# Kernel tuning notes

Hardware: AMD Instinct MI355X
Metric: run time of the kernel (lower is better)

The kernel has to match this reference:

```python
import jax, jax.numpy as jnp
import numpy as np

R = 32
GN_GROUPS = 8
GN_EPS = 1e-5


def group_norm(x, gamma, beta, groups=GN_GROUPS, eps=GN_EPS):
    B, C = x.shape[0], x.shape[1]
    sp = x.shape[2:]
    xg = x.reshape(B, groups, -1)
    mean = xg.mean(-1, keepdims=True)
    var = xg.var(-1, keepdims=True)
    xg = (xg - mean) * jax.lax.rsqrt(var + eps)
    x = xg.reshape((B, C) + sp)
    bshape = (1, C) + (1,) * len(sp)
    return x * gamma.reshape(bshape) + beta.reshape(bshape)


def swish(x):
    return x * jax.nn.sigmoid(x)


def voxelize_coords(coords, r):
    # coords: [B,3,N] -> normalized coords in [0, r-1]
    nc = coords - coords.mean(2, keepdims=True)
    scale = jnp.linalg.norm(nc, axis=1, keepdims=True).max(axis=2, keepdims=True) * 2.0
    nc = nc / scale + 0.5
    return jnp.clip(nc * r, 0.0, r - 1.0)


def avg_voxelize(features, vox, r):
    # features [B,C,N], vox int32 [B,3,N] -> [B,C,r,r,r] scatter-mean
    B, C, N = features.shape
    flat = (vox[:, 0] * r + vox[:, 1]) * r + vox[:, 2]          # [B,N]
    seg = (flat + jnp.arange(B, dtype=flat.dtype)[:, None] * (r ** 3)).reshape(-1)
    feats = features.transpose(0, 2, 1).reshape(B * N, C)
    sums = jax.ops.segment_sum(feats, seg, num_segments=B * r ** 3)
    cnts = jax.ops.segment_sum(jnp.ones((B * N,), features.dtype), seg,
                               num_segments=B * r ** 3)
    mean = sums / jnp.maximum(cnts, 1.0)[:, None]
    return mean.reshape(B, r, r, r, C).transpose(0, 4, 1, 2, 3)


def trilinear_devoxelize(grid, coords, r):
    # grid [B,C,r,r,r], coords float [B,3,N] in [0,r-1] -> [B,C,N]
    B, C = grid.shape[0], grid.shape[1]
    N = coords.shape[2]
    lo = jnp.floor(coords).astype(jnp.int32)                     # [B,3,N]
    frac = coords - lo.astype(coords.dtype)
    hi = jnp.minimum(lo + 1, r - 1)
    gridf = grid.reshape(B, C, r * r * r)
    out = jnp.zeros((B, C, N), grid.dtype)
    for dx in (0, 1):
        for dy in (0, 1):
            for dz in (0, 1):
                ix = hi[:, 0] if dx else lo[:, 0]
                iy = hi[:, 1] if dy else lo[:, 1]
                iz = hi[:, 2] if dz else lo[:, 2]
                wx = frac[:, 0] if dx else (1.0 - frac[:, 0])
                wy = frac[:, 1] if dy else (1.0 - frac[:, 1])
                wz = frac[:, 2] if dz else (1.0 - frac[:, 2])
                idx = (ix * r + iy) * r + iz                     # [B,N]
                g = jnp.take_along_axis(gridf,
                                        jnp.broadcast_to(idx[:, None, :], (B, C, N)),
                                        axis=2)
                out = out + (wx * wy * wz)[:, None, :] * g
    return out


def conv3d(x, w, b):
    y = jax.lax.conv_general_dilated(x, w, (1, 1, 1), 'SAME',
                                     dimension_numbers=('NCDHW', 'OIDHW', 'NCDHW'))
    return y + b.reshape(1, -1, 1, 1, 1)


def setup_inputs() -> dict:
    key = jax.random.key(0)
    ks = jax.random.split(key, 20)
    B, Cin, Cout, N, k = 8, 64, 128, 32768, 3
    red = Cout // 8  # SE reduction
    s = 0.05
    return {
        'features': jax.random.normal(ks[0], (B, Cin, N), jnp.float32),
        'coords':   jax.random.normal(ks[1], (B, 3, N), jnp.float32),
        'conv1_w': jax.random.normal(ks[2], (Cout, Cin, k, k, k), jnp.float32) * s,
        'conv1_b': jnp.zeros((Cout,), jnp.float32),
        'gn1_g': jnp.ones((Cout,), jnp.float32),
        'gn1_b': jnp.zeros((Cout,), jnp.float32),
        'conv2_w': jax.random.normal(ks[3], (Cout, Cout, k, k, k), jnp.float32) * s,
        'conv2_b': jnp.zeros((Cout,), jnp.float32),
        'gn2_g': jnp.ones((Cout,), jnp.float32),
        'gn2_b': jnp.zeros((Cout,), jnp.float32),
        'se_w1': jax.random.normal(ks[4], (red, Cout), jnp.float32) * s,
        'se_b1': jnp.zeros((red,), jnp.float32),
        'se_w2': jax.random.normal(ks[5], (Cout, red), jnp.float32) * s,
        'se_b2': jnp.zeros((Cout,), jnp.float32),
        'pt_w': jax.random.normal(ks[6], (Cout, Cin), jnp.float32) * s,
        'pt_b': jnp.zeros((Cout,), jnp.float32),
        'ptgn_g': jnp.ones((Cout,), jnp.float32),
        'ptgn_b': jnp.zeros((Cout,), jnp.float32),
    }


def reference(features, coords, conv1_w, conv1_b, gn1_g, gn1_b,
              conv2_w, conv2_b, gn2_g, gn2_b,
              se_w1, se_b1, se_w2, se_b2,
              pt_w, pt_b, ptgn_g, ptgn_b):
    # Voxelization (coords detached in original)
    c = jax.lax.stop_gradient(coords)
    norm_coords = voxelize_coords(c, R)                  # [B,3,N] float in [0,R-1]
    vox_coords = jnp.round(norm_coords).astype(jnp.int32)
    grid = avg_voxelize(features, vox_coords, R)         # [B,Cin,R,R,R]

    # voxel layers: conv -> GN -> swish -> (dropout=identity, eval) -> conv -> GN -> SE
    g = conv3d(grid, conv1_w, conv1_b)
    g = swish(group_norm(g, gn1_g, gn1_b))
    g = conv3d(g, conv2_w, conv2_b)
    g = group_norm(g, gn2_g, gn2_b)
    # SE3d
    s = g.mean((2, 3, 4))                                # [B,Cout]
    s = jax.nn.relu(s @ se_w1.T + se_b1)
    s = jax.nn.sigmoid(s @ se_w2.T + se_b2)
    g = g * s[:, :, None, None, None]

    voxel_feats = trilinear_devoxelize(g, norm_coords, R)  # [B,Cout,N]

    # point branch: SharedMLP = Conv1d(1x1) -> GN -> swish
    pt = jnp.einsum('oc,bcn->bon', pt_w, features) + pt_b[None, :, None]
    pt = swish(group_norm(pt, ptgn_g, ptgn_b))

    return voxel_feats + pt
```

## Files before the change

kernel.cpp:

```cpp
#include <hip/hip_runtime.h>
#include <cmath>

typedef unsigned short u16;
typedef unsigned int u32;
typedef __bf16 bf16x8 __attribute__((ext_vector_type(8)));
typedef float f32x4 __attribute__((ext_vector_type(4)));

__device__ __forceinline__ u16 f2bf(float f) {
  u32 u = __float_as_uint(f);
  u32 r = (u + 0x7FFFu + ((u >> 16) & 1u)) >> 16;
  return (u16)r;
}
__device__ __forceinline__ float bf2f(u32 h) { return __uint_as_float(h << 16); }
__device__ __forceinline__ float swishf(float y) { return y / (1.0f + __expf(-y)); }

__global__ void k_csum(const float* __restrict__ coords, float* __restrict__ cstat) {
  const int b = blockIdx.y, t = threadIdx.x;
  const int n0 = blockIdx.x * 1024;
  float s[3] = {0.f, 0.f, 0.f};
#pragma unroll
  for (int a = 0; a < 3; ++a) {
    const float* p = coords + (b * 3 + a) * 32768 + n0;
#pragma unroll
    for (int i = 0; i < 4; ++i) s[a] += p[t + i * 256];
  }
#pragma unroll
  for (int a = 0; a < 3; ++a) {
#pragma unroll
    for (int d = 1; d < 64; d <<= 1) s[a] += __shfl_xor(s[a], d);
    if ((t & 63) == 0) atomicAdd(&cstat[b * 4 + a], s[a]);
  }
}

__global__ void k_cmax(const float* __restrict__ coords, float* __restrict__ cstat) {
  const int b = blockIdx.y, t = threadIdx.x;
  const int n0 = blockIdx.x * 1024;
  const float mx = cstat[b * 4 + 0] * (1.0f / 32768.0f);
  const float my = cstat[b * 4 + 1] * (1.0f / 32768.0f);
  const float mz = cstat[b * 4 + 2] * (1.0f / 32768.0f);
  float mv = 0.f;
#pragma unroll
  for (int i = 0; i < 4; ++i) {
    const int n = n0 + t + i * 256;
    const float dx = coords[(b * 3 + 0) * 32768 + n] - mx;
    const float dy = coords[(b * 3 + 1) * 32768 + n] - my;
    const float dz = coords[(b * 3 + 2) * 32768 + n] - mz;
    mv = fmaxf(mv, dx * dx + dy * dy + dz * dz);
  }
#pragma unroll
  for (int d = 1; d < 64; d <<= 1) mv = fmaxf(mv, __shfl_xor(mv, d));
  if ((t & 63) == 0) atomicMax((u32*)&cstat[b * 4 + 3], __float_as_uint(sqrtf(mv)));
}

__global__ void k_count(const float* __restrict__ coords, const float* __restrict__ cstat,
                        float4* __restrict__ nrm, int* __restrict__ vid, int* __restrict__ hist) {
  const int idx = blockIdx.x * 256 + threadIdx.x;
  const int b = idx >> 15, n = idx & 32767;
  const float mx = cstat[b * 4 + 0] * (1.0f / 32768.0f);
  const float my = cstat[b * 4 + 1] * (1.0f / 32768.0f);
  const float mz = cstat[b * 4 + 2] * (1.0f / 32768.0f);
  const float mn = __uint_as_float(__float_as_uint(cstat[b * 4 + 3]));
  const float inv = 1.0f / (mn * 2.0f);
  float nx = ((coords[(b * 3 + 0) * 32768 + n] - mx) * inv + 0.5f) * 32.0f;
  float ny = ((coords[(b * 3 + 1) * 32768 + n] - my) * inv + 0.5f) * 32.0f;
  float nz = ((coords[(b * 3 + 2) * 32768 + n] - mz) * inv + 0.5f) * 32.0f;
  nx = fminf(fmaxf(nx, 0.0f), 31.0f);
  ny = fminf(fmaxf(ny, 0.0f), 31.0f);
  nz = fminf(fmaxf(nz, 0.0f), 31.0f);
  float4 o; o.x = nx; o.y = ny; o.z = nz; o.w = 0.f;
  nrm[idx] = o;
  const int v = (((int)rintf(nx)) << 10) + (((int)rintf(ny)) << 5) + (int)rintf(nz);
  vid[idx] = v;
  atomicAdd(&hist[(b << 15) + v], 1);
}

__launch_bounds__(1024)
__global__ void k_scan(const int* __restrict__ hist, int* __restrict__ start,
                       int* __restrict__ cursor) {
  const int b = blockIdx.x, t = threadIdx.x;
  __shared__ int sdata[1024];
  const int base = (b << 15) + t * 32;
  int h[32];
  int sum = 0;
#pragma unroll
  for (int i = 0; i < 32; ++i) {
    h[i] = hist[base + i];
    sum += h[i];
  }
  sdata[t] = sum;
  __syncthreads();
  for (int off = 1; off < 1024; off <<= 1) {
    int v = (t >= off) ? sdata[t - off] : 0;
    __syncthreads();
    sdata[t] += v;
    __syncthreads();
  }
  int run = sdata[t] - sum;
#pragma unroll
  for (int i = 0; i < 32; ++i) {
    start[base + i] = run;
    cursor[base + i] = run;
    run += h[i];
  }
}

__global__ void k_scatteridx(const int* __restrict__ vid, int* __restrict__ cursor,
                             int* __restrict__ order) {
  const int idx = blockIdx.x * 256 + threadIdx.x;
  const int b = idx >> 15, n = idx & 32767;
  const int v = vid[idx];
  const int pos = atomicAdd(&cursor[(b << 15) + v], 1);
  order[(b << 15) + pos] = n;
}

__global__ void k_transpose(const float* __restrict__ feat, float* __restrict__ featT) {
  __shared__ float tile[64][65];
  const int t = threadIdx.x;
  const int b = blockIdx.y;
  const int n0 = blockIdx.x << 6;
#pragma unroll
  for (int i = 0; i < 16; ++i) {
    const int li = i * 256 + t;
    const int c = li >> 6, n = li & 63;
    tile[n][c] = feat[((size_t)(b * 64 + c) << 15) + n0 + n];
  }
  __syncthreads();
#pragma unroll
  for (int i = 0; i < 16; ++i) {
    const int li = i * 256 + t;
    const int n = li >> 6, c = li & 63;
    featT[(((size_t)(b << 15) + n0 + n) << 6) + c] = tile[n][c];
  }
}

__launch_bounds__(256)
__global__ void k_gather(const float* __restrict__ featT, const int* __restrict__ order,
                         const int* __restrict__ start, u16* __restrict__ gb) {
  const int t = threadIdx.x;
  const int b = blockIdx.y;
  const int v = (blockIdx.x << 2) + (t >> 6);
  const int c = t & 63;
  const int s = start[(b << 15) + v];
  const int e = (v == 32767) ? 32768 : start[(b << 15) + v + 1];
  float acc = 0.f;
  for (int p = s; p < e; ++p) {
    const int n = order[(b << 15) + p];
    acc += featT[(((size_t)(b << 15) + n) << 6) + c];
  }
  const float inv = 1.0f / (float)max(e - s, 1);
  gb[(((size_t)(b << 15) + v) << 6) + c] = f2bf(acc * inv);
}

template <int CI>
__global__ void k_prepw(const float* __restrict__ w, u16* __restrict__ wr) {
  const int idx = blockIdx.x * 256 + threadIdx.x;
  if (idx >= 27 * 128 * CI) return;
  const int off = idx / (128 * CI);
  const int rem = idx - off * (128 * CI);
  const int co = rem / CI;
  const int ci = rem - co * CI;
  wr[idx] = f2bf(w[(co * CI + ci) * 27 + off]);
}

template <int CI>
__launch_bounds__(256, 2)
__global__ void k_conv(const u16* __restrict__ in, const u16* __restrict__ W,
                       const float* __restrict__ bias, u16* __restrict__ outp,
                       float* __restrict__ ssum, float* __restrict__ ssq) {
  constexpr int CIC = 40;
  __shared__ u16 lin[612 * CIC];
  const int t = threadIdx.x;
  const int wave = t >> 6, lane = t & 63;
  const int l15 = lane & 15, quad = lane >> 4;
  const int x0 = blockIdx.x << 2;
  const int y = blockIdx.y;
  const int b = blockIdx.z;
  const int mq = wave & 1, nq = wave >> 1;

  f32x4 acc[4][4];
#pragma unroll
  for (int i = 0; i < 4; ++i)
#pragma unroll
    for (int j = 0; j < 4; ++j) acc[i][j] = (f32x4)0.0f;

  for (int cc = 0; cc < CI / 32; ++cc) {
    __syncthreads();
    const int ci0 = cc << 5;
    for (int id = t; id < 2448; id += 256) {
      const int row = id >> 2, c16 = id & 3;
      const int xs = row / 102, rem = row - xs * 102;
      const int ys = rem / 34, zp = rem - ys * 34;
      const int x = x0 + xs - 1, yy = y + ys - 1, zz = zp - 1;
      uint4 val = make_uint4(0u, 0u, 0u, 0u);
      if ((u32)x < 32u && (u32)yy < 32u && (u32)zz < 32u)
        val = *(const uint4*)(in + (((b << 15) + (x << 10) + (yy << 5) + zz) * CI + ci0 + (c16 << 3)));
      *(uint4*)(lin + row * CIC + (c16 << 3)) = val;
    }
    __syncthreads();

#pragma unroll 1
    for (int off = 0; off < 27; ++off) {
      const int dx = off / 9, r9 = off - dx * 9;
      const int dy = r9 / 3, dz = r9 - dy * 3;
      bf16x8 af[4];
#pragma unroll
      for (int mt = 0; mt < 4; ++mt) {
        const int co = (mq << 6) + (mt << 4) + l15;
        af[mt] = *(const bf16x8*)(W + ((off << 7) + co) * CI + ci0 + (quad << 3));
      }
      bf16x8 bfr[4];
#pragma unroll
      for (int nt = 0; nt < 4; ++nt) {
        const int px = (nq << 1) + (nt >> 1);
        const int z = ((nt & 1) << 4) + l15;
        const int rowi = ((px + dx) * 3 + dy) * 34 + z + dz;
        bfr[nt] = *(const bf16x8*)(lin + rowi * CIC + (quad << 3));
      }
#pragma unroll
      for (int mt = 0; mt < 4; ++mt)
#pragma unroll
        for (int nt = 0; nt < 4; ++nt)
          acc[mt][nt] = __builtin_amdgcn_mfma_f32_16x16x32_bf16(af[mt], bfr[nt], acc[mt][nt], 0, 0, 0);
    }
  }

  float ps[16], pq[16];
#pragma unroll
  for (int i = 0; i < 16; ++i) { ps[i] = 0.f; pq[i] = 0.f; }
#pragma unroll
  for (int mt = 0; mt < 4; ++mt) {
    const int co0 = (mq << 6) + (mt << 4) + (quad << 2);
    const float4 b4 = *(const float4*)(bias + co0);
#pragma unroll
    for (int nt = 0; nt < 4; ++nt) {
      const int px = (nq << 1) + (nt >> 1);
      const int z = ((nt & 1) << 4) + l15;
      const int v = ((x0 + px) << 10) + (y << 5) + z;
      const float v0 = acc[mt][nt][0] + b4.x;
      const float v1 = acc[mt][nt][1] + b4.y;
      const float v2 = acc[mt][nt][2] + b4.z;
      const float v3 = acc[mt][nt][3] + b4.w;
      ps[mt * 4 + 0] += v0; pq[mt * 4 + 0] += v0 * v0;
      ps[mt * 4 + 1] += v1; pq[mt * 4 + 1] += v1 * v1;
      ps[mt * 4 + 2] += v2; pq[mt * 4 + 2] += v2 * v2;
      ps[mt * 4 + 3] += v3; pq[mt * 4 + 3] += v3 * v3;
      uint2 pk;
      pk.x = (u32)f2bf(v0) | ((u32)f2bf(v1) << 16);
      pk.y = (u32)f2bf(v2) | ((u32)f2bf(v3) << 16);
      *(uint2*)(outp + ((b << 15) + v) * 128 + co0) = pk;
    }
  }
#pragma unroll
  for (int i = 0; i < 16; ++i) {
#pragma unroll
    for (int d = 1; d < 16; d <<= 1) {
      ps[i] += __shfl_xor(ps[i], d);
      pq[i] += __shfl_xor(pq[i], d);
    }
  }
  if (l15 == 0) {
#pragma unroll
    for (int mt = 0; mt < 4; ++mt)
#pragma unroll
      for (int r = 0; r < 4; ++r) {
        const int co = (mq << 6) + (mt << 4) + (quad << 2) + r;
        atomicAdd(&ssum[b * 128 + co], ps[mt * 4 + r]);
        atomicAdd(&ssq[b * 128 + co], pq[mt * 4 + r]);
      }
  }
}

__global__ void k_gnaff(const float* __restrict__ s, const float* __restrict__ q,
                        const float* __restrict__ gg, const float* __restrict__ gb,
                        float* __restrict__ A, float* __restrict__ B) {
  const int b = blockIdx.x, c = threadIdx.x;
  __shared__ float gs[8], gq[8];
  if (c < 8) { gs[c] = 0.f; gq[c] = 0.f; }
  __syncthreads();
  const float sc = s[b * 128 + c], qc = q[b * 128 + c];
  atomicAdd(&gs[c >> 4], sc);
  atomicAdd(&gq[c >> 4], qc);
  __syncthreads();
  const float inv = 1.0f / 524288.0f;
  const float mg = gs[c >> 4] * inv;
  const float var = gq[c >> 4] * inv - mg * mg;
  const float rs = rsqrtf(var + 1e-5f);
  const float a = gg[c] * rs;
  A[b * 128 + c] = a;
  B[b * 128 + c] = gb[c] - mg * a;
}

__global__ void k_se(const float* __restrict__ s, const float* __restrict__ q,
                     const float* __restrict__ gg, const float* __restrict__ gb,
                     const float* __restrict__ w1, const float* __restrict__ b1,
                     const float* __restrict__ w2, const float* __restrict__ b2,
                     float* __restrict__ A, float* __restrict__ B) {
  const int b = blockIdx.x, c = threadIdx.x;
  __shared__ float gs[8], gq[8], sarr[128], h[16];
  if (c < 8) { gs[c] = 0.f; gq[c] = 0.f; }
  __syncthreads();
  const float sc = s[b * 128 + c], qc = q[b * 128 + c];
  atomicAdd(&gs[c >> 4], sc);
  atomicAdd(&gq[c >> 4], qc);
  __syncthreads();
  const float inv = 1.0f / 524288.0f;
  const float mg = gs[c >> 4] * inv;
  const float var = gq[c >> 4] * inv - mg * mg;
  const float rs = rsqrtf(var + 1e-5f);
  const float a = gg[c] * rs;
  const float bb = gb[c] - mg * a;
  sarr[c] = (sc * (1.0f / 32768.0f)) * a + bb;
  __syncthreads();
  if (c < 16) {
    float accv = b1[c];
    for (int i = 0; i < 128; ++i) accv += w1[c * 128 + i] * sarr[i];
    h[c] = fmaxf(accv, 0.f);
  }
  __syncthreads();
  float o = b2[c];
  for (int r = 0; r < 16; ++r) o += w2[c * 16 + r] * h[r];
  const float se = 1.0f / (1.0f + __expf(-o));
  A[b * 128 + c] = a * se;
  B[b * 128 + c] = bb * se;
}

__global__ void k_gnapply(const u16* __restrict__ x, const float* __restrict__ A,
                          const float* __restrict__ B, u16* __restrict__ outp) {
  const int idx = blockIdx.x * 256 + threadIdx.x;
  const int e0 = idx << 3;
  const int b = e0 >> 22;
  const int c0 = e0 & 127;
  const uint4 v = ((const uint4*)x)[idx];
  const float* Ab = A + b * 128 + c0;
  const float* Bb = B + b * 128 + c0;
  u32 vv[4] = {v.x, v.y, v.z, v.w};
  uint4 o;
  u32 rr[4];
#pragma unroll
  for (int i = 0; i < 4; ++i) {
    float y0 = bf2f(vv[i] & 0xffffu) * Ab[2 * i] + Bb[2 * i];
    float y1 = bf2f(vv[i] >> 16) * Ab[2 * i + 1] + Bb[2 * i + 1];
    y0 = swishf(y0);
    y1 = swishf(y1);
    rr[i] = (u32)f2bf(y0) | ((u32)f2bf(y1) << 16);
  }
  o.x = rr[0]; o.y = rr[1]; o.z = rr[2]; o.w = rr[3];
  ((uint4*)outp)[idx] = o;
}

__launch_bounds__(256, 2)
__global__ void k_pt(const float* __restrict__ feat, const float* __restrict__ pw,
                     const float* __restrict__ pb, float* __restrict__ outp,
                     float* __restrict__ ssum, float* __restrict__ ssq) {
  __shared__ float fl[64 * 64];
  __shared__ float wl[64 * 132];
  const int t = threadIdx.x;
  const int n0g = blockIdx.x << 6;
  const int b = blockIdx.y;
  for (int i = t; i < 1024; i += 256) {
    const int fi = i << 2;
    const int k = fi >> 6, n = fi & 63;
    *(float4*)(fl + fi) = *(const float4*)(feat + ((size_t)(b * 64 + k) << 15) + n0g + n);
  }
  for (int i = t; i < 8192; i += 256) {
    const int c = i >> 6, k = i & 63;
    wl[k * 132 + c] = pw[i];
  }
  __syncthreads();
  const int tc = t >> 3, tn = t & 7;
  const int c0 = tc << 2, n0 = tn << 3;
  float acc[4][8];
#pragma unroll
  for (int i = 0; i < 4; ++i)
#pragma unroll
    for (int j = 0; j < 8; ++j) acc[i][j] = 0.f;
#pragma unroll 4
  for (int k = 0; k < 64; ++k) {
    const float4 a4 = *(const float4*)(wl + k * 132 + c0);
    const float4 b0 = *(const float4*)(fl + (k << 6) + n0);
    const float4 b1 = *(const float4*)(fl + (k << 6) + n0 + 4);
    const float av[4] = {a4.x, a4.y, a4.z, a4.w};
    const float bv[8] = {b0.x, b0.y, b0.z, b0.w, b1.x, b1.y, b1.z, b1.w};
#pragma unroll
    for (int i = 0; i < 4; ++i)
#pragma unroll
      for (int j = 0; j < 8; ++j) acc[i][j] += av[i] * bv[j];
  }
#pragma unroll
  for (int i = 0; i < 4; ++i) {
    const int c = c0 + i;
    const float bias = pb[c];
    float s = 0.f, q = 0.f;
    float vv[8];
#pragma unroll
    for (int j = 0; j < 8; ++j) {
      vv[j] = acc[i][j] + bias;
      s += vv[j];
      q += vv[j] * vv[j];
    }
    float4 o0, o1;
    o0.x = vv[0]; o0.y = vv[1]; o0.z = vv[2]; o0.w = vv[3];
    o1.x = vv[4]; o1.y = vv[5]; o1.z = vv[6]; o1.w = vv[7];
    float* op = outp + (((size_t)(b * 128 + c)) << 15) + n0g + n0;
    *(float4*)op = o0;
    *(float4*)(op + 4) = o1;
    for (int d = 1; d < 8; d <<= 1) {
      s += __shfl_xor(s, d);
      q += __shfl_xor(q, d);
    }
    if (tn == 0) {
      atomicAdd(&ssum[b * 128 + c], s);
      atomicAdd(&ssq[b * 128 + c], q);
    }
  }
}

__launch_bounds__(256)
__global__ void k_devox(const u16* __restrict__ g, const float4* __restrict__ nrm,
                        const float* __restrict__ A2, const float* __restrict__ B2,
                        const float* __restrict__ A3, const float* __restrict__ B3,
                        float* __restrict__ outp) {
  __shared__ float tri[64][129];
  const int t = threadIdx.x;
  const int blk = blockIdx.x, b = blockIdx.y;
  {
    const int pl = t & 63, cg = t >> 6;
    const float4 nc = nrm[(b << 15) + blk * 64 + pl];
    const int ix0 = (int)floorf(nc.x), iy0 = (int)floorf(nc.y), iz0 = (int)floorf(nc.z);
    const float rx = nc.x - (float)ix0, ry = nc.y - (float)iy0, rz = nc.z - (float)iz0;
    const int ix1 = min(ix0 + 1, 31), iy1 = min(iy0 + 1, 31), iz1 = min(iz0 + 1, 31);
    float acc[32];
#pragma unroll
    for (int i = 0; i < 32; ++i) acc[i] = 0.f;
    for (int cr = 0; cr < 8; ++cr) {
      const int xx = (cr & 4) ? ix1 : ix0;
      const int yv = (cr & 2) ? iy1 : iy0;
      const int zv = (cr & 1) ? iz1 : iz0;
      const float w = ((cr & 4) ? rx : 1.f - rx) * ((cr & 2) ? ry : 1.f - ry) *
                      ((cr & 1) ? rz : 1.f - rz);
      const uint4* src =
          (const uint4*)(g + ((size_t)((b << 15) + (xx << 10) + (yv << 5) + zv) << 7) + (cg << 5));
#pragma unroll
      for (int qq = 0; qq < 4; ++qq) {
        const uint4 u = src[qq];
        acc[qq * 8 + 0] += w * bf2f(u.x & 0xffffu);
        acc[qq * 8 + 1] += w * bf2f(u.x >> 16);
        acc[qq * 8 + 2] += w * bf2f(u.y & 0xffffu);
        acc[qq * 8 + 3] += w * bf2f(u.y >> 16);
        acc[qq * 8 + 4] += w * bf2f(u.z & 0xffffu);
        acc[qq * 8 + 5] += w * bf2f(u.z >> 16);
        acc[qq * 8 + 6] += w * bf2f(u.w & 0xffffu);
        acc[qq * 8 + 7] += w * bf2f(u.w >> 16);
      }
    }
    const int cb = b * 128 + (cg << 5);
#pragma unroll
    for (int i = 0; i < 32; ++i) tri[pl][(cg << 5) + i] = acc[i] * A2[cb + i] + B2[cb + i];
  }
  __syncthreads();
  {
    const int nl = t & 63, cg = t >> 6;
#pragma unroll 4
    for (int i = 0; i < 32; ++i) {
      const int c = (cg << 5) + i;
      const size_t oi = (((size_t)(b * 128 + c)) << 15) + blk * 64 + nl;
      const float pv = outp[oi];
      const float y = pv * A3[b * 128 + c] + B3[b * 128 + c];
      outp[oi] = tri[nl][c] + swishf(y);
    }
  }
}

extern "C" void kernel_launch(void* const* d_in, const int* in_sizes, int n_in,
                              void* d_out, int out_size, void* d_ws, size_t ws_size,
                              hipStream_t stream) {
  const float* features = (const float*)d_in[0];
  const float* coords = (const float*)d_in[1];
  const float* conv1_w = (const float*)d_in[2];
  const float* conv1_b = (const float*)d_in[3];
  const float* gn1_g = (const float*)d_in[4];
  const float* gn1_b = (const float*)d_in[5];
  const float* conv2_w = (const float*)d_in[6];
  const float* conv2_b = (const float*)d_in[7];
  const float* gn2_g = (const float*)d_in[8];
  const float* gn2_b = (const float*)d_in[9];
  const float* se_w1 = (const float*)d_in[10];
  const float* se_b1 = (const float*)d_in[11];
  const float* se_w2 = (const float*)d_in[12];
  const float* se_b2 = (const float*)d_in[13];
  const float* pt_w = (const float*)d_in[14];
  const float* pt_b = (const float*)d_in[15];
  const float* ptgn_g = (const float*)d_in[16];
  const float* ptgn_b = (const float*)d_in[17];

  char* ws = (char*)d_ws;
  float* cstat = (float*)ws;
  float* s1 = cstat + 32;
  float* q1 = s1 + 1024;
  float* s2 = q1 + 1024;
  float* q2 = s2 + 1024;
  float* s3 = q2 + 1024;
  float* q3 = s3 + 1024;
  float* A1 = q3 + 1024;
  float* B1 = A1 + 1024;
  float* A2 = B1 + 1024;
  float* B2 = A2 + 1024;
  float* A3 = B2 + 1024;
  float* B3 = A3 + 1024;
  size_t o = 65536;
  u16* Wr1 = (u16*)(ws + o); o += (size_t)27 * 128 * 64 * 2;
  u16* Wr2 = (u16*)(ws + o); o += (size_t)27 * 128 * 128 * 2;
  o = (o + 255) & ~(size_t)255;
  float4* nrm = (float4*)(ws + o); o += (size_t)8 * 32768 * 16;
  char* regA = ws + o; o += (size_t)8 * 32768 * 128 * 2;
  u16* gridbf = (u16*)(ws + o); o += (size_t)8 * 32768 * 64 * 2;
  u16* c2in = (u16*)(ws + o); o += (size_t)8 * 32768 * 128 * 2;
  int* vid = (int*)(ws + o); o += (size_t)8 * 32768 * 4;
  int* hist = (int*)(ws + o); o += (size_t)8 * 32768 * 4;
  int* startb = (int*)(ws + o); o += (size_t)8 * 32768 * 4;
  int* cursor = (int*)(ws + o); o += (size_t)8 * 32768 * 4;
  int* order = (int*)(ws + o); o += (size_t)8 * 32768 * 4;
  float* featT = (float*)regA;
  u16* c1raw = (u16*)regA;
  u16* c2raw = (u16*)regA;

  hipMemsetAsync(cstat, 0, 65536, stream);
  hipMemsetAsync(hist, 0, (size_t)8 * 32768 * 4, stream);

  k_prepw<64><<<dim3((27 * 128 * 64 + 255) / 256), 256, 0, stream>>>(conv1_w, Wr1);
  k_prepw<128><<<dim3((27 * 128 * 128 + 255) / 256), 256, 0, stream>>>(conv2_w, Wr2);
  k_csum<<<dim3(32, 8), 256, 0, stream>>>(coords, cstat);
  k_cmax<<<dim3(32, 8), 256, 0, stream>>>(coords, cstat);
  k_count<<<1024, 256, 0, stream>>>(coords, cstat, nrm, vid, hist);
  k_scan<<<8, 1024, 0, stream>>>(hist, startb, cursor);
  k_scatteridx<<<1024, 256, 0, stream>>>(vid, cursor, order);
  k_transpose<<<dim3(512, 8), 256, 0, stream>>>(features, featT);
  k_gather<<<dim3(8192, 8), 256, 0, stream>>>(featT, order, startb, gridbf);
  k_conv<64><<<dim3(8, 32, 8), 256, 0, stream>>>(gridbf, Wr1, conv1_b, c1raw, s1, q1);
  k_gnaff<<<8, 128, 0, stream>>>(s1, q1, gn1_g, gn1_b, A1, B1);
  k_gnapply<<<16384, 256, 0, stream>>>(c1raw, A1, B1, c2in);
  k_conv<128><<<dim3(8, 32, 8), 256, 0, stream>>>(c2in, Wr2, conv2_b, c2raw, s2, q2);
  k_pt<<<dim3(512, 8), 256, 0, stream>>>(features, pt_w, pt_b, (float*)d_out, s3, q3);
  k_se<<<8, 128, 0, stream>>>(s2, q2, gn2_g, gn2_b, se_w1, se_b1, se_w2, se_b2, A2, B2);
  k_gnaff<<<8, 128, 0, stream>>>(s3, q3, ptgn_g, ptgn_b, A3, B3);
  k_devox<<<dim3(512, 8), 256, 0, stream>>>(c2raw, nrm, A2, B2, A3, B3, (float*)d_out);
}
```

Before: 1.749 ms.

## Fuse GroupNorm+swish into conv2 input load and double-buffer conv fragment loads

Removes the separate GN-apply+swish kernel and applies the per-channel affine and swish inside conv2 while it stages the input tile into LDS. This avoids writing and re-reading a 64 MB bf16 intermediate. The conv inner loop is also restructured so the weight and LDS fragments for the next offset load while the MFMAs for the current one run, using two register sets. The cost is that halo voxels are recomputed across neighbouring blocks, plus higher register pressure.

```diff
diff --git a/kernel.cpp b/kernel.cpp
--- a/kernel.cpp
+++ b/kernel.cpp
@@ -162,11 +162,13 @@
   wr[idx] = f2bf(w[(co * CI + ci) * 27 + off]);
 }
 
-template <int CI>
+template <int CI, bool FUSE>
 __launch_bounds__(256, 2)
 __global__ void k_conv(const u16* __restrict__ in, const u16* __restrict__ W,
-                       const float* __restrict__ bias, u16* __restrict__ outp,
-                       float* __restrict__ ssum, float* __restrict__ ssq) {
+                       const float* __restrict__ bias,
+                       const float* __restrict__ Apre, const float* __restrict__ Bpre,
+                       u16* __restrict__ outp, float* __restrict__ ssum,
+                       float* __restrict__ ssq) {
   constexpr int CIC = 40;
   __shared__ u16 lin[612 * CIC];
   const int t = threadIdx.x;
@@ -183,45 +185,92 @@
 #pragma unroll
     for (int j = 0; j < 4; ++j) acc[i][j] = (f32x4)0.0f;
 
+  int badr[4];
+#pragma unroll
+  for (int nt = 0; nt < 4; ++nt) {
+    const int px = (nq << 1) + (nt >> 1);
+    const int z = ((nt & 1) << 4) + l15;
+    badr[nt] = (px * 3 * 34 + z) * CIC + (quad << 3);
+  }
+
   for (int cc = 0; cc < CI / 32; ++cc) {
+    const int ci0 = cc << 5;
+    float aV[8], bV[8];
+    if (FUSE) {
+      const int chb = b * 128 + ci0 + (t & 3) * 8;
+#pragma unroll
+      for (int j = 0; j < 8; ++j) {
+        aV[j] = Apre[chb + j];
+        bV[j] = Bpre[chb + j];
+      }
+    }
     __syncthreads();
-    const int ci0 = cc << 5;
     for (int id = t; id < 2448; id += 256) {
       const int row = id >> 2, c16 = id & 3;
       const int xs = row / 102, rem = row - xs * 102;
       const int ys = rem / 34, zp = rem - ys * 34;
       const int x = x0 + xs - 1, yy = y + ys - 1, zz = zp - 1;
       uint4 val = make_uint4(0u, 0u, 0u, 0u);
-      if ((u32)x < 32u && (u32)yy < 32u && (u32)zz < 32u)
+      if ((u32)x < 32u && (u32)yy < 32u && (u32)zz < 32u) {
         val = *(const uint4*)(in + (((b << 15) + (x << 10) + (yy << 5) + zz) * CI + ci0 + (c16 << 3)));
+        if (FUSE) {
+          u32 w4[4] = {val.x, val.y, val.z, val.w};
+#pragma unroll
+          for (int j = 0; j < 4; ++j) {
+            float y0 = bf2f(w4[j] & 0xffffu) * aV[2 * j] + bV[2 * j];
+            float y1 = bf2f(w4[j] >> 16) * aV[2 * j + 1] + bV[2 * j + 1];
+            y0 = swishf(y0);
+            y1 = swishf(y1);
+            w4[j] = (u32)f2bf(y0) | ((u32)f2bf(y1) << 16);
+          }
+          val.x = w4[0]; val.y = w4[1]; val.z = w4[2]; val.w = w4[3];
+        }
+      }
       *(uint4*)(lin + row * CIC + (c16 << 3)) = val;
     }
     __syncthreads();
 
+    const u16* wA = W + ((mq << 6) + l15) * CI + ci0 + (quad << 3);
+
+    bf16x8 afA[4], bfA[4], afB[4], bfB[4];
+
+#define LOADF(OFF, AF, BF)                                                  \
+  {                                                                         \
+    const int _o = (OFF);                                                   \
+    const int _dx = _o / 9, _rr = _o - _dx * 9;                             \
+    const int _dy = _rr / 3, _dz = _rr - _dy * 3;                           \
+    const int _ro = (_dx * 102 + _dy * 34 + _dz) * CIC;                     \
+    const u16* _wp = wA + (size_t)_o * (128 * CI);                          \
+    AF[0] = *(const bf16x8*)(_wp);                                          \
+    AF[1] = *(const bf16x8*)(_wp + 16 * CI);                                \
+    AF[2] = *(const bf16x8*)(_wp + 32 * CI);                                \
+    AF[3] = *(const bf16x8*)(_wp + 48 * CI);                                \
+    BF[0] = *(const bf16x8*)(lin + badr[0] + _ro);                          \
+    BF[1] = *(const bf16x8*)(lin + badr[1] + _ro);                          \
+    BF[2] = *(const bf16x8*)(lin + badr[2] + _ro);                          \
+    BF[3] = *(const bf16x8*)(lin + badr[3] + _ro);                          \
+  }
+
+#define MFMAS(AF, BF)                                                       \
+  {                                                                         \
+    _Pragma("unroll") for (int mt = 0; mt < 4; ++mt)                        \
+        _Pragma("unroll") for (int nt = 0; nt < 4; ++nt) acc[mt][nt] =      \
+            __builtin_amdgcn_mfma_f32_16x16x32_bf16(AF[mt], BF[nt],         \
+                                                    acc[mt][nt], 0, 0, 0);  \
+  }
+
+    LOADF(0, afA, bfA);
 #pragma unroll 1
-    for (int off = 0; off < 27; ++off) {
-      const int dx = off / 9, r9 = off - dx * 9;
-      const int dy = r9 / 3, dz = r9 - dy * 3;
-      bf16x8 af[4];
-#pragma unroll
-      for (int mt = 0; mt < 4; ++mt) {
-        const int co = (mq << 6) + (mt << 4) + l15;
-        af[mt] = *(const bf16x8*)(W + ((off << 7) + co) * CI + ci0 + (quad << 3));
-      }
-      bf16x8 bfr[4];
-#pragma unroll
-      for (int nt = 0; nt < 4; ++nt) {
-        const int px = (nq << 1) + (nt >> 1);
-        const int z = ((nt & 1) << 4) + l15;
-        const int rowi = ((px + dx) * 3 + dy) * 34 + z + dz;
-        bfr[nt] = *(const bf16x8*)(lin + rowi * CIC + (quad << 3));
-      }
-#pragma unroll
-      for (int mt = 0; mt < 4; ++mt)
-#pragma unroll
-        for (int nt = 0; nt < 4; ++nt)
-          acc[mt][nt] = __builtin_amdgcn_mfma_f32_16x16x32_bf16(af[mt], bfr[nt], acc[mt][nt], 0, 0, 0);
-    }
+    for (int op = 0; op < 13; ++op) {
+      const int o2 = op << 1;
+      LOADF(o2 + 1, afB, bfB);
+      MFMAS(afA, bfA);
+      LOADF(o2 + 2, afA, bfA);
+      MFMAS(afB, bfB);
+    }
+    MFMAS(afA, bfA);
+#undef LOADF
+#undef MFMAS
   }
 
   float ps[16], pq[16];
@@ -322,30 +371,6 @@
   const float se = 1.0f / (1.0f + __expf(-o));
   A[b * 128 + c] = a * se;
   B[b * 128 + c] = bb * se;
-}
-
-__global__ void k_gnapply(const u16* __restrict__ x, const float* __restrict__ A,
-                          const float* __restrict__ B, u16* __restrict__ outp) {
-  const int idx = blockIdx.x * 256 + threadIdx.x;
-  const int e0 = idx << 3;
-  const int b = e0 >> 22;
-  const int c0 = e0 & 127;
-  const uint4 v = ((const uint4*)x)[idx];
-  const float* Ab = A + b * 128 + c0;
-  const float* Bb = B + b * 128 + c0;
-  u32 vv[4] = {v.x, v.y, v.z, v.w};
-  uint4 o;
-  u32 rr[4];
-#pragma unroll
-  for (int i = 0; i < 4; ++i) {
-    float y0 = bf2f(vv[i] & 0xffffu) * Ab[2 * i] + Bb[2 * i];
-    float y1 = bf2f(vv[i] >> 16) * Ab[2 * i + 1] + Bb[2 * i + 1];
-    y0 = swishf(y0);
-    y1 = swishf(y1);
-    rr[i] = (u32)f2bf(y0) | ((u32)f2bf(y1) << 16);
-  }
-  o.x = rr[0]; o.y = rr[1]; o.z = rr[2]; o.w = rr[3];
-  ((uint4*)outp)[idx] = o;
 }
 
 __launch_bounds__(256, 2)
@@ -514,14 +539,13 @@
   float4* nrm = (float4*)(ws + o); o += (size_t)8 * 32768 * 16;
   char* regA = ws + o; o += (size_t)8 * 32768 * 128 * 2;
   u16* gridbf = (u16*)(ws + o); o += (size_t)8 * 32768 * 64 * 2;
-  u16* c2in = (u16*)(ws + o); o += (size_t)8 * 32768 * 128 * 2;
+  u16* c1raw = (u16*)(ws + o); o += (size_t)8 * 32768 * 128 * 2;
   int* vid = (int*)(ws + o); o += (size_t)8 * 32768 * 4;
   int* hist = (int*)(ws + o); o += (size_t)8 * 32768 * 4;
   int* startb = (int*)(ws + o); o += (size_t)8 * 32768 * 4;
   int* cursor = (int*)(ws + o); o += (size_t)8 * 32768 * 4;
   int* order = (int*)(ws + o); o += (size_t)8 * 32768 * 4;
   float* featT = (float*)regA;
-  u16* c1raw = (u16*)regA;
   u16* c2raw = (u16*)regA;
 
   hipMemsetAsync(cstat, 0, 65536, stream);
@@ -536,10 +560,11 @@
   k_scatteridx<<<1024, 256, 0, stream>>>(vid, cursor, order);
   k_transpose<<<dim3(512, 8), 256, 0, stream>>>(features, featT);
   k_gather<<<dim3(8192, 8), 256, 0, stream>>>(featT, order, startb, gridbf);
-  k_conv<64><<<dim3(8, 32, 8), 256, 0, stream>>>(gridbf, Wr1, conv1_b, c1raw, s1, q1);
+  k_conv<64, false><<<dim3(8, 32, 8), 256, 0, stream>>>(gridbf, Wr1, conv1_b, nullptr, nullptr,
+                                                        c1raw, s1, q1);
   k_gnaff<<<8, 128, 0, stream>>>(s1, q1, gn1_g, gn1_b, A1, B1);
-  k_gnapply<<<16384, 256, 0, stream>>>(c1raw, A1, B1, c2in);
-  k_conv<128><<<dim3(8, 32, 8), 256, 0, stream>>>(c2in, Wr2, conv2_b, c2raw, s2, q2);
+  k_conv<128, true><<<dim3(8, 32, 8), 256, 0, stream>>>(c1raw, Wr2, conv2_b, A1, B1,
+                                                        c2raw, s2, q2);
   k_pt<<<dim3(512, 8), 256, 0, stream>>>(features, pt_w, pt_b, (float*)d_out, s3, q3);
   k_se<<<8, 128, 0, stream>>>(s2, q2, gn2_g, gn2_b, se_w1, se_b1, se_w2, se_b2, A2, B2);
   k_gnaff<<<8, 128, 0, stream>>>(s3, q3, ptgn_g, ptgn_b, A3, B3);
```

New measurement: 1.627 ms. 1.07x faster.
